# Kernel tuning notes

Hardware: AMD Instinct MI355X
Metric: run time of the kernel (lower is better)

## Reference

```python
import jax, jax.numpy as jnp
import numpy as np

N_NODES = 50000
N_EDGES = 800000
IN_C, OUT_C, EDGE_F, HEADS, HID, FINAL = 8, 16, 8, 4, 64, 128
NEG_SLOPE = 0.2  # PyG GATConv default LeakyReLU slope


def setup_inputs() -> dict:
    key = jax.random.key(0)
    ks = jax.random.split(key, 12)
    s = 0.1
    return {
        "x": jax.random.normal(ks[0], (N_NODES, IN_C), jnp.float32),
        "edge_index": jax.random.randint(ks[1], (2, N_EDGES), 0, N_NODES, jnp.int64),
        "edge_attr": jax.random.normal(ks[2], (N_EDGES, EDGE_F), jnp.float32),
        # NNConv params: root weight, bias, edge-MLP Linear(EDGE_F -> IN_C*OUT_C)
        "ecc_root": jax.random.normal(ks[3], (IN_C, OUT_C), jnp.float32) * s,
        "ecc_bias": jnp.zeros((OUT_C,), jnp.float32),
        "mlp_w": jax.random.normal(ks[4], (EDGE_F, IN_C * OUT_C), jnp.float32) * s,
        "mlp_b": jnp.zeros((IN_C * OUT_C,), jnp.float32),
        # GATConv params
        "gat_lin": jax.random.normal(ks[5], (OUT_C, HEADS * HID), jnp.float32) * s,
        "att_src": jax.random.normal(ks[6], (HEADS, HID), jnp.float32) * s,
        "att_dst": jax.random.normal(ks[7], (HEADS, HID), jnp.float32) * s,
        "gat_bias": jnp.zeros((HEADS * HID,), jnp.float32),
        # final Linear
        "fc_w": jax.random.normal(ks[8], (HEADS * HID, FINAL), jnp.float32) * s,
        "fc_b": jnp.zeros((FINAL,), jnp.float32),
    }


def _forward(x, edge_index, edge_attr, ecc_root, ecc_bias, mlp_w, mlp_b,
             gat_lin, att_src, att_dst, gat_bias, fc_w, fc_b):
    src, dst = edge_index[0], edge_index[1]  # messages flow src -> dst

    # ---- NNConv (edge-conditioned conv), aggr='add' ----
    # per-edge weight matrices [E, IN_C, OUT_C] from edge MLP
    w_e = (edge_attr @ mlp_w + mlp_b).reshape(-1, IN_C, OUT_C)
    msg = jnp.einsum('ei,eio->eo', x[src], w_e)                 # [E, OUT_C]
    agg = jax.ops.segment_sum(msg, dst, num_segments=N_NODES)   # [N, OUT_C]
    h = jax.nn.relu(x @ ecc_root + agg + ecc_bias)              # [N, OUT_C]

    # ---- GATConv (heads concatenated) ----
    g = (h @ gat_lin).reshape(N_NODES, HEADS, HID)              # [N, H, D]
    a_src = jnp.einsum('nhd,hd->nh', g, att_src)                # [N, H]
    a_dst = jnp.einsum('nhd,hd->nh', g, att_dst)
    e = jax.nn.leaky_relu(a_src[src] + a_dst[dst], NEG_SLOPE)   # [E, H]
    # segment softmax over incoming edges of each dst node
    e_max = jax.ops.segment_max(e, dst, num_segments=N_NODES)   # [N, H]
    e_max = jnp.where(jnp.isfinite(e_max), e_max, 0.0)
    e_exp = jnp.exp(e - e_max[dst])                             # [E, H]
    denom = jax.ops.segment_sum(e_exp, dst, num_segments=N_NODES)
    alpha = e_exp / (denom[dst] + 1e-16)                        # [E, H]
    out = jax.ops.segment_sum(alpha[:, :, None] * g[src], dst,
                              num_segments=N_NODES)             # [N, H, D]
    out = jax.nn.relu(out.reshape(N_NODES, HEADS * HID) + gat_bias)

    # ---- final linear ----
    return out @ fc_w + fc_b                                    # [N, FINAL]


def reference(x, edge_index, edge_attr, ecc_root, ecc_bias, mlp_w, mlp_b,
              gat_lin, att_src, att_dst, gat_bias, fc_w, fc_b):
    return _forward(x, edge_index, edge_attr, ecc_root, ecc_bias, mlp_w, mlp_b,
                    gat_lin, att_src, att_dst, gat_bias, fc_w, fc_b)
```

## Files before the change

kernel.cpp:

```cpp
#include <hip/hip_runtime.h>

#define N_NODES 50000
#define N_EDGES 800000
#define IN_C 8
#define OUT_C 16
#define EDGE_F 8
#define HEADS 4
#define HID 64
#define GDIM (HEADS*HID)
#define FINAL 128
#define NEG_SLOPE 0.2f
#define EB ((N_EDGES+255)/256)
#define NBLK 196

__device__ __forceinline__ int clampn(int v) {
    return v < 0 ? 0 : (v >= N_NODES ? N_NODES - 1 : v);
}

__global__ __launch_bounds__(256) void k_histfold(
    const int* __restrict__ dst, int* __restrict__ cnt, int* __restrict__ rnk,
    const float* __restrict__ gat_lin,
    const float* __restrict__ att_src_w, const float* __restrict__ att_dst_w,
    float* __restrict__ wsrc, float* __restrict__ wdst)
{
    if (blockIdx.x < EB) {
        int e = blockIdx.x * 256 + threadIdx.x;
        if (e >= N_EDGES) return;
        rnk[e] = atomicAdd(&cnt[clampn(dst[e])], 1);
    } else {
        int t = threadIdx.x;
        if (t >= 64) return;
        int c = t >> 2, h = t & 3;
        float ws = 0.f, wd = 0.f;
        for (int k = 0; k < HID; k++) {
            float l = gat_lin[c * GDIM + h * HID + k];
            ws += l * att_src_w[h * HID + k];
            wd += l * att_dst_w[h * HID + k];
        }
        wsrc[t] = ws;
        wdst[t] = wd;
    }
}

__global__ __launch_bounds__(256) void k_part(const int* __restrict__ cnt,
                                              int* __restrict__ part)
{
    int i = blockIdx.x * 256 + threadIdx.x;
    int v = (i < N_NODES) ? cnt[i] : 0;
#pragma unroll
    for (int off = 32; off; off >>= 1) v += __shfl_down(v, off);
    __shared__ int ws[4];
    if ((threadIdx.x & 63) == 0) ws[threadIdx.x >> 6] = v;
    __syncthreads();
    if (threadIdx.x == 0) part[blockIdx.x] = ws[0] + ws[1] + ws[2] + ws[3];
}

__global__ __launch_bounds__(256) void k_scan1(const int* __restrict__ part,
                                               int* __restrict__ partscan)
{
    int t = threadIdx.x;
    int v = (t < NBLK) ? part[t] : 0;
    int lane = t & 63, wid = t >> 6;
    int incl = v;
#pragma unroll
    for (int off = 1; off < 64; off <<= 1) {
        int u = __shfl_up(incl, off);
        if (lane >= off) incl += u;
    }
    __shared__ int wsum[4];
    if (lane == 63) wsum[wid] = incl;
    __syncthreads();
    int add = 0;
    for (int w = 0; w < wid; w++) add += wsum[w];
    partscan[t] = incl - v + add;
}

__global__ __launch_bounds__(256) void k_add(const int* __restrict__ cnt,
                                             const int* __restrict__ partscan,
                                             int* __restrict__ offs)
{
    int i = blockIdx.x * 256 + threadIdx.x;
    int v = (i < N_NODES) ? cnt[i] : 0;
    int lane = threadIdx.x & 63, wid = threadIdx.x >> 6;
    int incl = v;
#pragma unroll
    for (int off = 1; off < 64; off <<= 1) {
        int u = __shfl_up(incl, off);
        if (lane >= off) incl += u;
    }
    __shared__ int wsum[4];
    if (lane == 63) wsum[wid] = incl;
    __syncthreads();
    int add = partscan[blockIdx.x];
    for (int w = 0; w < wid; w++) add += wsum[w];
    if (i < N_NODES) offs[i] = incl - v + add;
    if (i == 0) offs[N_NODES] = N_EDGES;
}

__global__ __launch_bounds__(256) void k_scatter(
    const int* __restrict__ src, const int* __restrict__ dst,
    const int* __restrict__ rnk, const int* __restrict__ offs,
    const float* __restrict__ ea,
    int* __restrict__ src_csr, float* __restrict__ ea_csr)
{
    int e = blockIdx.x * 256 + threadIdx.x;
    if (e >= N_EDGES) return;
    int p = offs[clampn(dst[e])] + rnk[e];
    src_csr[p] = clampn(src[e]);
    const float4* s4 = (const float4*)&ea[(size_t)e * EDGE_F];
    float4* d4 = (float4*)&ea_csr[(size_t)p * EDGE_F];
    d4[0] = s4[0];
    d4[1] = s4[1];
}

__global__ __launch_bounds__(256) void k2T_wave(
    const float* __restrict__ x,
    const int* __restrict__ src_csr, const int* __restrict__ offs,
    const float* __restrict__ ea_csr,
    const float* __restrict__ mlp_w, const float* __restrict__ mlp_b,
    const float* __restrict__ ecc_root, const float* __restrict__ ecc_bias,
    const float* __restrict__ wsrc, const float* __restrict__ wdst,
    float* __restrict__ h_tab, float* __restrict__ asrc, float* __restrict__ adst)
{
    __shared__ float smW[64 * 17];
    __shared__ float smb[128];
    __shared__ float sroot[128];
    __shared__ float sbias[16];
    __shared__ float sws[64], swd[64];
    __shared__ float sT[4][64];
    __shared__ float sxs[4][8];

    int t = threadIdx.x;
    for (int idx = t; idx < 1024; idx += 256)
        smW[(idx >> 4) * 17 + (idx & 15)] = mlp_w[idx];
    if (t < 128) smb[t] = mlp_b[t];
    if (t >= 128 && t < 256) sroot[t - 128] = ecc_root[t - 128];
    if (t < 16) sbias[t] = ecc_bias[t];
    if (t >= 32 && t < 96) sws[t - 32] = wsrc[t - 32];
    if (t >= 96 && t < 160) swd[t - 96] = wdst[t - 96];

    int wid = t >> 6, lane = t & 63;
    int n = blockIdx.x * 4 + wid;
    int f = lane >> 3, i = lane & 7;
    int beg = offs[n], end = offs[n + 1];

    float t0 = 0.f, t1 = 0.f, t2 = 0.f, t3 = 0.f, xs = 0.f;
    int j = beg;
    for (; j + 3 < end; j += 4) {
        int s0 = src_csr[j],     s1 = src_csr[j + 1];
        int s2 = src_csr[j + 2], s3 = src_csr[j + 3];
        float a0 = ea_csr[(size_t)j * EDGE_F + f];
        float a1 = ea_csr[(size_t)(j + 1) * EDGE_F + f];
        float a2 = ea_csr[(size_t)(j + 2) * EDGE_F + f];
        float a3 = ea_csr[(size_t)(j + 3) * EDGE_F + f];
        float x0 = x[s0 * IN_C + i];
        float x1 = x[s1 * IN_C + i];
        float x2 = x[s2 * IN_C + i];
        float x3 = x[s3 * IN_C + i];
        t0 += a0 * x0; t1 += a1 * x1; t2 += a2 * x2; t3 += a3 * x3;
        xs += (x0 + x1) + (x2 + x3);
    }
    for (; j < end; j++) {
        int s = src_csr[j];
        float a = ea_csr[(size_t)j * EDGE_F + f];
        float xv = x[s * IN_C + i];
        t0 += a * xv;
        xs += xv;
    }
    sT[wid][lane] = (t0 + t1) + (t2 + t3);
    if (f == 0) sxs[wid][i] = xs;
    __syncthreads();

    int o = lane & 15, p = lane >> 4;
    float v = 0.f;
#pragma unroll
    for (int q2 = 0; q2 < 16; q2++) {
        int jj = p * 16 + q2;
        v += smW[jj * 17 + o] * sT[wid][jj];
    }
    v += __shfl_down(v, 32);
    v += __shfl_down(v, 16);

    float hv = 0.f;
    if (lane < 16) {
        float vv = v + sbias[o];
#pragma unroll
        for (int ii = 0; ii < IN_C; ii++) {
            vv += smb[ii * 16 + o] * sxs[wid][ii];
            vv += x[n * IN_C + ii] * sroot[ii * 16 + o];
        }
        hv = fmaxf(vv, 0.f);
        h_tab[n * OUT_C + o] = hv;
    }
    float as = 0.f, ad = 0.f;
    int h2 = lane & 3;
#pragma unroll
    for (int c = 0; c < 16; c++) {
        float hc = __shfl(hv, c);
        as += hc * sws[c * 4 + h2];
        ad += hc * swd[c * 4 + h2];
    }
    if (lane < 4) {
        asrc[n * HEADS + lane] = as;
        adst[n * HEADS + lane] = ad;
    }
}

__global__ __launch_bounds__(256) void k_gatE(
    const int* __restrict__ offs, const int* __restrict__ src_csr,
    const float* __restrict__ asrc, const float* __restrict__ adst,
    const float* __restrict__ h_tab, float* __restrict__ U_all)
{
    int t = threadIdx.x;
    int wid = t >> 6, lane = t & 63;
    int n = blockIdx.x * 4 + wid;
    int h = lane >> 4, c = lane & 15;
    float adsth = adst[n * HEADS + h];
    int beg = offs[n], end = offs[n + 1];

    float U = 0.f, den = 0.f;
    int j = beg;
    for (; j + 3 < end; j += 4) {
        int s0 = src_csr[j],     s1 = src_csr[j + 1];
        int s2 = src_csr[j + 2], s3 = src_csr[j + 3];
        float av0 = asrc[s0 * HEADS + h], av1 = asrc[s1 * HEADS + h];
        float av2 = asrc[s2 * HEADS + h], av3 = asrc[s3 * HEADS + h];
        float h0 = h_tab[s0 * OUT_C + c], h1 = h_tab[s1 * OUT_C + c];
        float h2v = h_tab[s2 * OUT_C + c], h3v = h_tab[s3 * OUT_C + c];
        float v0 = av0 + adsth; v0 = v0 > 0.f ? v0 : NEG_SLOPE * v0;
        float v1 = av1 + adsth; v1 = v1 > 0.f ? v1 : NEG_SLOPE * v1;
        float v2 = av2 + adsth; v2 = v2 > 0.f ? v2 : NEG_SLOPE * v2;
        float v3 = av3 + adsth; v3 = v3 > 0.f ? v3 : NEG_SLOPE * v3;
        float p0 = __expf(v0), p1 = __expf(v1), p2 = __expf(v2), p3 = __expf(v3);
        den += (p0 + p1) + (p2 + p3);
        U += p0 * h0 + p1 * h1 + p2 * h2v + p3 * h3v;
    }
    for (; j < end; j++) {
        int s = src_csr[j];
        float av = asrc[s * HEADS + h];
        float hvv = h_tab[s * OUT_C + c];
        float v = av + adsth; v = v > 0.f ? v : NEG_SLOPE * v;
        float pe = __expf(v);
        den += pe;
        U += pe * hvv;
    }
    U_all[(size_t)n * 64 + lane] = U / (den + 1e-16f);
}

#define FBM 32
__global__ __launch_bounds__(256) void k_fuse(
    const float* __restrict__ U_all, const float* __restrict__ gat_lin,
    const float* __restrict__ gat_bias, const float* __restrict__ fc_w,
    const float* __restrict__ fc_b, float* __restrict__ y)
{
    __shared__ float sA[16][FBM + 4];
    __shared__ float sW[16][64];
    int tid = threadIdx.x;
    int r0 = blockIdx.x * FBM;

    int ar  = tid >> 3;
    int ak  = (tid & 7) * 2;
    int grow = r0 + ar;

    int w    = tid >> 6;
    int lane = tid & 63;
    int trow = (w >> 1) * 16 + (lane >> 4) * 4;
    int tcol = (w & 1) * 64 + (lane & 15) * 4;
    bool useLds = ((w & 1) == 0);

    int skk = tid >> 4;
    int scc = (tid & 15) * 4;

    float acc[4][4];
#pragma unroll
    for (int r = 0; r < 4; r++)
#pragma unroll
        for (int c = 0; c < 4; c++) acc[r][c] = 0.f;

    for (int h = 0; h < HEADS; ++h) {
        float4 ua = make_float4(0.f, 0.f, 0.f, 0.f), ub = ua, uc4 = ua, ud = ua;
        if (grow < N_NODES) {
            const float4* up = (const float4*)&U_all[(size_t)grow * 64 + h * 16];
            ua = up[0]; ub = up[1]; uc4 = up[2]; ud = up[3];
        }
        float ureg[16] = {ua.x, ua.y, ua.z, ua.w,  ub.x, ub.y, ub.z, ub.w,
                          uc4.x, uc4.y, uc4.z, uc4.w,  ud.x, ud.y, ud.z, ud.w};

#pragma unroll
        for (int tt = 0; tt < 4; ++tt) {
            int k0 = h * 64 + tt * 16;
            float b0 = gat_bias[k0 + ak];
            float b1 = gat_bias[k0 + ak + 1];
            float g0 = 0.f, g1 = 0.f;
#pragma unroll
            for (int c = 0; c < 16; ++c) {
                const float* lp = &gat_lin[c * GDIM + k0 + ak];
                g0 += ureg[c] * lp[0];
                g1 += ureg[c] * lp[1];
            }
            __syncthreads();
            sA[ak][ar]     = fmaxf(g0 + b0, 0.f);
            sA[ak + 1][ar] = fmaxf(g1 + b1, 0.f);
            *(float4*)&sW[skk][scc] =
                *(const float4*)&fc_w[(size_t)(k0 + skk) * FINAL + scc];
            __syncthreads();

            if (useLds) {
#pragma unroll
                for (int kk = 0; kk < 16; ++kk) {
                    float4 wv = *(const float4*)&sW[kk][tcol];
                    float4 a = *(const float4*)&sA[kk][trow];
                    float av[4] = {a.x, a.y, a.z, a.w};
#pragma unroll
                    for (int r = 0; r < 4; r++) {
                        acc[r][0] += av[r] * wv.x;
                        acc[r][1] += av[r] * wv.y;
                        acc[r][2] += av[r] * wv.z;
                        acc[r][3] += av[r] * wv.w;
                    }
                }
            } else {
#pragma unroll
                for (int kk = 0; kk < 16; ++kk) {
                    float4 wv = *(const float4*)&fc_w[(size_t)(k0 + kk) * FINAL + tcol];
                    float4 a = *(const float4*)&sA[kk][trow];
                    float av[4] = {a.x, a.y, a.z, a.w};
#pragma unroll
                    for (int r = 0; r < 4; r++) {
                        acc[r][0] += av[r] * wv.x;
                        acc[r][1] += av[r] * wv.y;
                        acc[r][2] += av[r] * wv.z;
                        acc[r][3] += av[r] * wv.w;
                    }
                }
            }
        }
    }

    float4 fb = *(const float4*)&fc_b[tcol];
#pragma unroll
    for (int r = 0; r < 4; r++) {
        int row = r0 + trow + r;
        if (row < N_NODES) {
            *(float4*)&y[(size_t)row * FINAL + tcol] =
                make_float4(acc[r][0] + fb.x, acc[r][1] + fb.y,
                            acc[r][2] + fb.z, acc[r][3] + fb.w);
        }
    }
}

extern "C" void kernel_launch(void* const* d_in, const int* in_sizes, int n_in,
                              void* d_out, int out_size, void* d_ws, size_t ws_size,
                              hipStream_t stream)
{
    const float* x        = (const float*)d_in[0];
    const int*   ei       = (const int*)d_in[1];
    const float* ea       = (const float*)d_in[2];
    const float* ecc_root = (const float*)d_in[3];
    const float* ecc_bias = (const float*)d_in[4];
    const float* mlp_w    = (const float*)d_in[5];
    const float* mlp_b    = (const float*)d_in[6];
    const float* gat_lin  = (const float*)d_in[7];
    const float* att_src  = (const float*)d_in[8];
    const float* att_dst  = (const float*)d_in[9];
    const float* gat_bias = (const float*)d_in[10];
    const float* fc_w     = (const float*)d_in[11];
    const float* fc_b     = (const float*)d_in[12];
    float* y = (float*)d_out;

    const int* src = ei;
    const int* dst = ei + N_EDGES;

    float* h_tab = (float*)d_ws;
    float* U_all = h_tab + (size_t)N_NODES * OUT_C;
    float* asrc  = U_all + (size_t)N_NODES * 64;
    float* adst  = asrc + (size_t)N_NODES * HEADS;
    float* wsrc  = adst + (size_t)N_NODES * HEADS;
    float* wdst  = wsrc + 64;
    int*   cnt      = (int*)(wdst + 64);
    int*   offs     = cnt + N_NODES;
    int*   part     = offs + N_NODES + 4;
    int*   partscan = part + 256;
    int*   rnk      = partscan + 256;
    int*   src_csr  = rnk + N_EDGES;
    float* ea_csr   = (float*)(src_csr + N_EDGES);

    hipMemsetAsync(cnt, 0, sizeof(int) * N_NODES, stream);

    k_histfold<<<EB + 1, 256, 0, stream>>>(dst, cnt, rnk, gat_lin, att_src, att_dst,
                                           wsrc, wdst);
    k_part    <<<NBLK, 256, 0, stream>>>(cnt, part);
    k_scan1   <<<1, 256, 0, stream>>>(part, partscan);
    k_add     <<<NBLK, 256, 0, stream>>>(cnt, partscan, offs);
    k_scatter <<<EB, 256, 0, stream>>>(src, dst, rnk, offs, ea, src_csr, ea_csr);

    k2T_wave  <<<N_NODES / 4, 256, 0, stream>>>(x, src_csr, offs, ea_csr, mlp_w, mlp_b,
                                                ecc_root, ecc_bias, wsrc, wdst,
                                                h_tab, asrc, adst);
    k_gatE    <<<N_NODES / 4, 256, 0, stream>>>(offs, src_csr, asrc, adst, h_tab, U_all);
    k_fuse    <<<(N_NODES + FBM - 1) / FBM, 256, 0, stream>>>(U_all, gat_lin, gat_bias,
                                                              fc_w, fc_b, y);
}
```

Baseline: 384.1 us.

## Retile fused GAT-linear kernel to 128 threads with gat_lin staged in LDS

The fused output kernel now runs 128 threads per block. Each thread accumulates a 4x8 output tile, and all fc_w reads go through LDS, replacing the old split where half the waves read global memory. The full gat_lin matrix (16x256) is copied into shared memory once per block, and each thread computes four hidden values with float4 LDS loads. The goal is fewer redundant global loads and less divergence between waves. The cost is more LDS per block, a load prologue in every block, and half as many threads to hide latency.

```diff
diff --git a/kernel.cpp b/kernel.cpp
--- a/kernel.cpp
+++ b/kernel.cpp
@@ -248,34 +248,36 @@
 }
 
 #define FBM 32
-__global__ __launch_bounds__(256) void k_fuse(
+__global__ __launch_bounds__(128) void k_fuse(
     const float* __restrict__ U_all, const float* __restrict__ gat_lin,
     const float* __restrict__ gat_bias, const float* __restrict__ fc_w,
     const float* __restrict__ fc_b, float* __restrict__ y)
 {
+    __shared__ float slin[16 * GDIM];
     __shared__ float sA[16][FBM + 4];
-    __shared__ float sW[16][64];
+    __shared__ float sW[16][FINAL];
     int tid = threadIdx.x;
     int r0 = blockIdx.x * FBM;
 
-    int ar  = tid >> 3;
-    int ak  = (tid & 7) * 2;
+    for (int idx = tid; idx < (16 * GDIM) / 4; idx += 128)
+        ((float4*)slin)[idx] = ((const float4*)gat_lin)[idx];
+    __syncthreads();
+
+    int ar  = tid >> 2;
+    int akq = (tid & 3) * 4;
     int grow = r0 + ar;
 
-    int w    = tid >> 6;
-    int lane = tid & 63;
-    int trow = (w >> 1) * 16 + (lane >> 4) * 4;
-    int tcol = (w & 1) * 64 + (lane & 15) * 4;
-    bool useLds = ((w & 1) == 0);
-
-    int skk = tid >> 4;
-    int scc = (tid & 15) * 4;
-
-    float acc[4][4];
+    int rg = tid >> 4;
+    int cg = tid & 15;
+
+    int skk = tid >> 3;
+    int scc = (tid & 7) * 16;
+
+    float acc[4][8];
 #pragma unroll
     for (int r = 0; r < 4; r++)
 #pragma unroll
-        for (int c = 0; c < 4; c++) acc[r][c] = 0.f;
+        for (int c = 0; c < 8; c++) acc[r][c] = 0.f;
 
     for (int h = 0; h < HEADS; ++h) {
         float4 ua = make_float4(0.f, 0.f, 0.f, 0.f), ub = ua, uc4 = ua, ud = ua;
@@ -289,62 +291,63 @@
 #pragma unroll
         for (int tt = 0; tt < 4; ++tt) {
             int k0 = h * 64 + tt * 16;
-            float b0 = gat_bias[k0 + ak];
-            float b1 = gat_bias[k0 + ak + 1];
-            float g0 = 0.f, g1 = 0.f;
+            float4 bv = *(const float4*)&gat_bias[k0 + akq];
+            float g0 = 0.f, g1 = 0.f, g2 = 0.f, g3 = 0.f;
 #pragma unroll
             for (int c = 0; c < 16; ++c) {
-                const float* lp = &gat_lin[c * GDIM + k0 + ak];
-                g0 += ureg[c] * lp[0];
-                g1 += ureg[c] * lp[1];
+                float4 lv = *(const float4*)&slin[c * GDIM + k0 + akq];
+                g0 += ureg[c] * lv.x;
+                g1 += ureg[c] * lv.y;
+                g2 += ureg[c] * lv.z;
+                g3 += ureg[c] * lv.w;
             }
             __syncthreads();
-            sA[ak][ar]     = fmaxf(g0 + b0, 0.f);
-            sA[ak + 1][ar] = fmaxf(g1 + b1, 0.f);
-            *(float4*)&sW[skk][scc] =
-                *(const float4*)&fc_w[(size_t)(k0 + skk) * FINAL + scc];
+            sA[akq + 0][ar] = fmaxf(g0 + bv.x, 0.f);
+            sA[akq + 1][ar] = fmaxf(g1 + bv.y, 0.f);
+            sA[akq + 2][ar] = fmaxf(g2 + bv.z, 0.f);
+            sA[akq + 3][ar] = fmaxf(g3 + bv.w, 0.f);
+            {
+                const float4* wsrc4 =
+                    (const float4*)&fc_w[(size_t)(k0 + skk) * FINAL + scc];
+                float4* wdst4 = (float4*)&sW[skk][scc];
+                wdst4[0] = wsrc4[0];
+                wdst4[1] = wsrc4[1];
+                wdst4[2] = wsrc4[2];
+                wdst4[3] = wsrc4[3];
+            }
             __syncthreads();
-
-            if (useLds) {
-#pragma unroll
-                for (int kk = 0; kk < 16; ++kk) {
-                    float4 wv = *(const float4*)&sW[kk][tcol];
-                    float4 a = *(const float4*)&sA[kk][trow];
-                    float av[4] = {a.x, a.y, a.z, a.w};
-#pragma unroll
-                    for (int r = 0; r < 4; r++) {
-                        acc[r][0] += av[r] * wv.x;
-                        acc[r][1] += av[r] * wv.y;
-                        acc[r][2] += av[r] * wv.z;
-                        acc[r][3] += av[r] * wv.w;
-                    }
-                }
-            } else {
-#pragma unroll
-                for (int kk = 0; kk < 16; ++kk) {
-                    float4 wv = *(const float4*)&fc_w[(size_t)(k0 + kk) * FINAL + tcol];
-                    float4 a = *(const float4*)&sA[kk][trow];
-                    float av[4] = {a.x, a.y, a.z, a.w};
-#pragma unroll
-                    for (int r = 0; r < 4; r++) {
-                        acc[r][0] += av[r] * wv.x;
-                        acc[r][1] += av[r] * wv.y;
-                        acc[r][2] += av[r] * wv.z;
-                        acc[r][3] += av[r] * wv.w;
-                    }
+#pragma unroll
+            for (int kk = 0; kk < 16; ++kk) {
+                float4 a  = *(const float4*)&sA[kk][rg * 4];
+                float4 w0 = *(const float4*)&sW[kk][cg * 8];
+                float4 w1 = *(const float4*)&sW[kk][cg * 8 + 4];
+                float av[4] = {a.x, a.y, a.z, a.w};
+#pragma unroll
+                for (int r = 0; r < 4; r++) {
+                    acc[r][0] += av[r] * w0.x;
+                    acc[r][1] += av[r] * w0.y;
+                    acc[r][2] += av[r] * w0.z;
+                    acc[r][3] += av[r] * w0.w;
+                    acc[r][4] += av[r] * w1.x;
+                    acc[r][5] += av[r] * w1.y;
+                    acc[r][6] += av[r] * w1.z;
+                    acc[r][7] += av[r] * w1.w;
                 }
             }
         }
     }
 
-    float4 fb = *(const float4*)&fc_b[tcol];
+    float4 fb0 = *(const float4*)&fc_b[cg * 8];
+    float4 fb1 = *(const float4*)&fc_b[cg * 8 + 4];
 #pragma unroll
     for (int r = 0; r < 4; r++) {
-        int row = r0 + trow + r;
+        int row = r0 + rg * 4 + r;
         if (row < N_NODES) {
-            *(float4*)&y[(size_t)row * FINAL + tcol] =
-                make_float4(acc[r][0] + fb.x, acc[r][1] + fb.y,
-                            acc[r][2] + fb.z, acc[r][3] + fb.w);
+            float* yp = &y[(size_t)row * FINAL + cg * 8];
+            *(float4*)&yp[0] = make_float4(acc[r][0] + fb0.x, acc[r][1] + fb0.y,
+                                           acc[r][2] + fb0.z, acc[r][3] + fb0.w);
+            *(float4*)&yp[4] = make_float4(acc[r][4] + fb1.x, acc[r][5] + fb1.y,
+                                           acc[r][6] + fb1.z, acc[r][7] + fb1.w);
         }
     }
 }
@@ -398,6 +401,6 @@
                                                 ecc_root, ecc_bias, wsrc, wdst,
                                                 h_tab, asrc, adst);
     k_gatE    <<<N_NODES / 4, 256, 0, stream>>>(offs, src_csr, asrc, adst, h_tab, U_all);
-    k_fuse    <<<(N_NODES + FBM - 1) / FBM, 256, 0, stream>>>(U_all, gat_lin, gat_bias,
+    k_fuse    <<<(N_NODES + FBM - 1) / FBM, 128, 0, stream>>>(U_all, gat_lin, gat_bias,
                                                               fc_w, fc_b, y);
 }
```

Result: faster. 351.8 us (-8.4%).
